# Kernel optimization log

Hardware: AMD Instinct MI355X
Metric: run time of the kernel (lower is better)

The kernel has to match this reference:

```python
import jax, jax.numpy as jnp
import numpy as np

B, T, H, IN = 256, 1024, 512, 1

def setup_inputs() -> dict:
    key = jax.random.key(0)
    ks = jax.random.split(key, 10)
    s = 1.0 / np.sqrt(H)
    return {
        "input": jax.random.normal(ks[0], (B, T), dtype=jnp.float32),
        "Wx0": jax.random.uniform(ks[1], (IN, 4 * H), jnp.float32, -s, s),
        "Wh0": jax.random.uniform(ks[2], (H, 4 * H), jnp.float32, -s, s),
        "b0": jax.random.uniform(ks[3], (4 * H,), jnp.float32, -s, s),
        "Wx1": jax.random.uniform(ks[4], (H, 4 * H), jnp.float32, -s, s),
        "Wh1": jax.random.uniform(ks[5], (H, 4 * H), jnp.float32, -s, s),
        "b1": jax.random.uniform(ks[6], (4 * H,), jnp.float32, -s, s),
        "Wf": jax.random.uniform(ks[7], (H, 1), jnp.float32, -s, s),
        "bf": jax.random.uniform(ks[8], (1,), jnp.float32, -s, s),
    }

def _lstm_layer(xs, Wx, Wh, b):
    # xs: [T, B, in] -> hs: [T, B, H]
    Bd = xs.shape[1]
    Hd = Wh.shape[0]
    h0 = jnp.zeros((Bd, Hd), xs.dtype)
    c0 = jnp.zeros((Bd, Hd), xs.dtype)
    def step(carry, x_t):
        h, c = carry
        g = x_t @ Wx + h @ Wh + b                     # [B, 4H]
        i, f, gg, o = jnp.split(g, 4, axis=-1)
        i = jax.nn.sigmoid(i)
        f = jax.nn.sigmoid(f)
        gg = jnp.tanh(gg)
        o = jax.nn.sigmoid(o)
        c_n = f * c + i * gg
        h_n = o * jnp.tanh(c_n)
        return (h_n, c_n), h_n
    _, hs = jax.lax.scan(step, (h0, c0), xs)
    return hs

def reference(input, Wx0, Wh0, b0, Wx1, Wh1, b1, Wf, bf):
    # input: [B, T] scalar sequence (input_size = 1)
    xs = input.T[:, :, None]                           # [T, B, 1]
    h1 = _lstm_layer(xs, Wx0, Wh0, b0)                 # [T, B, H]
    h2 = _lstm_layer(h1, Wx1, Wh1, b1)                 # [T, B, H]
    out = h2 @ Wf + bf                                 # [T, B, 1]
    return out[:, :, 0].T                              # [B, T]
```

## Files before the change

kernel.cpp:

```cpp
#include <hip/hip_runtime.h>


typedef _Float16 f16;
typedef _Float16 f16x8 __attribute__((ext_vector_type(8)));
typedef float f32x4 __attribute__((ext_vector_type(4)));
typedef unsigned long long u64;

#define NB 256
#define NT_ 1024
#define NH 512
#define RING 16
#define SLOT (NB * NH)

__device__ __forceinline__ float sigm(float x)  { return 1.0f / (1.0f + __expf(-x)); }
__device__ __forceinline__ float tanhx(float x) { return 2.0f / (1.0f + __expf(-2.0f * x)) - 1.0f; }

__device__ __forceinline__ void st8(unsigned short* p, u64 v) {
  __hip_atomic_store((u64*)p, v, __ATOMIC_RELAXED, __HIP_MEMORY_SCOPE_AGENT);
}
__device__ __forceinline__ unsigned ldf(const unsigned* p) {
  return __hip_atomic_load(p, __ATOMIC_RELAXED, __HIP_MEMORY_SCOPE_AGENT);
}
__device__ __forceinline__ unsigned pollr(const unsigned* a, unsigned thr) {
  unsigned v;
  for (;;) {
    v = ldf(a);
    if (!~__ballot(v >= thr)) break;
    __builtin_amdgcn_s_sleep(2);
  }
  asm volatile("" ::: "memory");
  return v;
}

__global__ void prep_xT(const float* __restrict__ inp, float* __restrict__ xT) {
  int g = blockIdx.x * 256 + threadIdx.x;
  int t = g >> 8, b = g & 255;
  xT[t * NB + b] = inp[b * NT_ + t];
}

__global__ void prep_w(const float* __restrict__ Wh0,
                       const float* __restrict__ Wx1,
                       const float* __restrict__ Wh1,
                       f16* __restrict__ dst) {
  int g = blockIdx.x * 256 + threadIdx.x;
  int mat = g >> 20;
  int r = g & 0xFFFFF;
  int j = r & 7, ln = (r >> 3) & 63, kt = (r >> 9) & 15;
  int cl = ln & 15, qd = ln >> 4;
  int k = kt * 32 + qd * 8 + j;
  size_t di; int gcol; const float* W;
  if (mat == 0) {
    int gt = (r >> 13) & 3, nh = (r >> 15) & 1, sl = (r >> 16) & 15;
    W = Wh0;
    gcol = gt * 512 + sl * 32 + nh * 16 + cl;
    di = (size_t)sl * 65536 + (((size_t)(nh * 4 + gt) * 16 + kt) * 64 + ln) * 8 + j;
  } else {
    int jt = (r >> 13) & 1, nh = (r >> 14) & 1, sl = (r >> 15) & 31;
    W = (mat == 1) ? Wx1 : Wh1;
    int gate = jt * 2 + (cl >> 3);
    gcol = gate * 512 + sl * 16 + nh * 8 + (cl & 7);
    di = (size_t)mat * 1048576 + (size_t)sl * 32768 +
         (((size_t)(nh * 2 + jt) * 16 + kt) * 64 + ln) * 8 + j;
  }
  dst[di] = (f16)W[(size_t)k * 2048 + gcol];
}

__global__ void reduce_out(const float* __restrict__ part8,
                           const float* __restrict__ bfp,
                           float* __restrict__ out) {
  int g = blockIdx.x * 256 + threadIdx.x;
  float v = bfp[0];
#pragma unroll
  for (int j = 0; j < 8; ++j) v += part8[(size_t)j * (NB * NT_) + g];
  out[g] = v;
}

__global__ __launch_bounds__(256, 1) void lstm_main(
    const float* __restrict__ xT,
    const f16*  __restrict__ wsl,
    const float* __restrict__ wx0,
    const float* __restrict__ bias0,
    const float* __restrict__ bias1,
    const float* __restrict__ wf,
    unsigned short* p_hi, unsigned short* p_lo,
    unsigned short* q_hi, unsigned short* q_lo,
    unsigned int* pf,
    unsigned int* qf,
    float* part8)
{
  extern __shared__ char smem[];
  const int tid = threadIdx.x;
  const int wv = tid >> 6, ln = tid & 63;
  const int qd = ln >> 4, cl = ln & 15;
  const int bx = blockIdx.x;
  const int r8 = bx & 7, idx = bx >> 3;
  const bool isL0 = !(r8 & 1);
  const int c = r8 >> 1;
  const int sl = idx;
  if (isL0 && idx >= 16) return;
  const float LO = 1.0f / 1024.0f;

  if (isL0) {
    const int4* s0 = (const int4*)wsl + (size_t)sl * 8192;
    int4* d = (int4*)smem;
    for (int i = tid; i < 8192; i += 256) d[i] = s0[i];
  } else {
    const int4* s1 = (const int4*)wsl + 131072 + (size_t)sl * 4096;
    const int4* s2 = (const int4*)wsl + 262144 + (size_t)sl * 4096;
    int4* d = (int4*)smem;
    for (int i = tid; i < 4096; i += 256) { d[i] = s1[i]; d[4096 + i] = s2[i]; }
  }
  __syncthreads();

  unsigned* pfc = pf + c * 32;
  unsigned* qfc = qf + c * 32;

  if (isL0) {
    const int nh = wv >> 1, rhalf = wv & 1;
    const int rb0 = c * 64 + rhalf * 32;
    float wx0v[4], b0c[4];
#pragma unroll
    for (int g = 0; g < 4; ++g) {
      int gc = g * 512 + sl * 32 + nh * 16 + cl;
      wx0v[g] = wx0[gc];
      b0c[g] = bias0[gc];
    }
    float cst[2][4] = {{0.f,0.f,0.f,0.f},{0.f,0.f,0.f,0.f}};
    const bool isq = (ln >= 16 && ln < 48);
    const unsigned* pwa = isq ? (qfc + (ln & 31)) : (pfc + (ln & 15));
    const f16x8* wl = (const f16x8*)smem;
    f16* sh  = (f16*)(smem + 131072);
    f16* slo = sh + 2048;

    for (int s = 0; s < NT_; ++s) {
      if ((s & (RING - 1)) == 0 && s) {
        __syncthreads();
        if (wv == 0)
          asm volatile("buffer_inv sc1\n\ts_waitcnt vmcnt(0)" ::: "memory");
        __syncthreads();
      }
      const int slot_r = (s + RING - 1) & (RING - 1);
      const int slot_w = s & (RING - 1);
      float4 xv[2];
#pragma unroll
      for (int rt = 0; rt < 2; ++rt)
        xv[rt] = *(const float4*)(xT + s * NB + rb0 + rt * 16 + qd * 4);
      if (s) {
        unsigned thr = isq ? (s >= RING ? (unsigned)(s - RING + 1) : 0u)
                           : (unsigned)s;
        pollr(pwa, thr);
      }
      f16x8 Ah[16][2], Al[16][2];
      {
        const f16* bh = (const f16*)p_hi + (size_t)slot_r * SLOT + (size_t)c * 32768 + qd * 8;
        const f16* bl = (const f16*)p_lo + (size_t)slot_r * SLOT + (size_t)c * 32768 + qd * 8;
#pragma unroll
        for (int kt = 0; kt < 16; ++kt)
#pragma unroll
          for (int rt = 0; rt < 2; ++rt) {
            int lr = rhalf * 32 + rt * 16 + cl;
            size_t off = (size_t)kt * 2048 + lr * 32;
            Ah[kt][rt] = *(const f16x8*)(bh + off);
            Al[kt][rt] = *(const f16x8*)(bl + off);
          }
      }
      f32x4 acc[4][2], accL[4][2];
#pragma unroll
      for (int g = 0; g < 4; ++g)
#pragma unroll
        for (int rt = 0; rt < 2; ++rt) {
          acc[g][rt] = (f32x4){0.f,0.f,0.f,0.f};
          accL[g][rt] = (f32x4){0.f,0.f,0.f,0.f};
        }
#pragma unroll
      for (int kt = 0; kt < 16; ++kt) {
#pragma unroll
        for (int g = 0; g < 4; ++g) {
          f16x8 bw = wl[((nh * 4 + g) * 16 + kt) * 64 + ln];
#pragma unroll
          for (int rt = 0; rt < 2; ++rt) {
            acc[g][rt]  = __builtin_amdgcn_mfma_f32_16x16x32_f16(Ah[kt][rt], bw, acc[g][rt], 0, 0, 0);
            accL[g][rt] = __builtin_amdgcn_mfma_f32_16x16x32_f16(Al[kt][rt], bw, accL[g][rt], 0, 0, 0);
          }
        }
      }
#pragma unroll
      for (int rt = 0; rt < 2; ++rt)
#pragma unroll
        for (int e = 0; e < 4; ++e) {
          float xe = (e == 0) ? xv[rt].x : (e == 1) ? xv[rt].y : (e == 2) ? xv[rt].z : xv[rt].w;
          float gi = acc[0][rt][e] + accL[0][rt][e] * LO + xe * wx0v[0] + b0c[0];
          float gf = acc[1][rt][e] + accL[1][rt][e] * LO + xe * wx0v[1] + b0c[1];
          float gg = acc[2][rt][e] + accL[2][rt][e] * LO + xe * wx0v[2] + b0c[2];
          float go = acc[3][rt][e] + accL[3][rt][e] * LO + xe * wx0v[3] + b0c[3];
          float ii = sigm(gi), ff = sigm(gf), tg = tanhx(gg), oo = sigm(go);
          cst[rt][e] = ff * cst[rt][e] + ii * tg;
          float h = oo * tanhx(cst[rt][e]);
          f16 hh = (f16)h;
          int su = (rhalf * 32 + rt * 16 + qd * 4 + e) * 32 + nh * 16 + cl;
          sh[su]  = hh;
          slo[su] = (f16)((h - (float)hh) * 1024.0f);
        }
      __syncthreads();
      {
        unsigned short* bh = p_hi + (size_t)slot_w * SLOT + (size_t)c * 32768 + (size_t)sl * 2048;
        unsigned short* bl = p_lo + (size_t)slot_w * SLOT + (size_t)c * 32768 + (size_t)sl * 2048;
#pragma unroll
        for (int i = tid; i < 1024; i += 256) {
          int strm = i >> 9, pc = i & 511;
          const f16* src = (strm ? slo : sh) + pc * 4;
          st8((strm ? bl : bh) + pc * 4, *(const u64*)src);
        }
      }
      __syncthreads();
      if (tid == 0)
        __hip_atomic_store(pfc + sl, (unsigned)(s + 1),
                           __ATOMIC_RELAXED, __HIP_MEMORY_SCOPE_AGENT);
    }
  } else {
    int u = cl & 7, g01 = cl >> 3;
    const bool hiH = (cl < 8);
    float b1c0[2], b1c1[2], wfv[2];
#pragma unroll
    for (int nh = 0; nh < 2; ++nh) {
      int base = sl * 16 + nh * 8 + u;
      b1c0[nh] = bias1[g01 * 512 + base];
      b1c1[nh] = bias1[(2 + g01) * 512 + base];
      wfv[nh] = wf[base];
    }
    const int lr = wv * 16 + cl;
    float cst[2][4] = {{0.f,0.f,0.f,0.f},{0.f,0.f,0.f,0.f}};
    unsigned pf_seen = 0;
    const f16x8* wx_ = (const f16x8*)smem;
    const f16x8* wh_ = (const f16x8*)(smem + 65536);
    f16* sh  = (f16*)(smem + 131072);
    f16* slo = sh + 1024;

    for (int s = 0; s < NT_; ++s) {
      if ((s & (RING - 1)) == 0 && s) {
        __syncthreads();
        if (wv == 0)
          asm volatile("buffer_inv sc1\n\ts_waitcnt vmcnt(0)" ::: "memory");
        __syncthreads();
      }
      const int slot_r = (s + RING - 1) & (RING - 1);
      const int slot_w = s & (RING - 1);
      if (s) pollr(qfc + (ln & 31), (unsigned)s);
      const f16* aqh = (const f16*)q_hi + (size_t)slot_r * SLOT + (size_t)c * 32768 +
                       (qd >> 1) * 1024 + lr * 16 + (qd & 1) * 8;
      const f16* aql = (const f16*)q_lo + (size_t)slot_r * SLOT + (size_t)c * 32768 +
                       (qd >> 1) * 1024 + lr * 16 + (qd & 1) * 8;
      f16x8 Aq[16][2];
#pragma unroll
      for (int kt = 0; kt < 16; ++kt) {
        Aq[kt][0] = *(const f16x8*)(aqh + kt * 2048);
        Aq[kt][1] = *(const f16x8*)(aql + kt * 2048);
      }
      const f16* aph = (const f16*)p_hi + (size_t)slot_w * SLOT + (size_t)c * 32768 +
                       lr * 32 + qd * 8;
      const f16* apl = (const f16*)p_lo + (size_t)slot_w * SLOT + (size_t)c * 32768 +
                       lr * 32 + qd * 8;
      bool early = __all((int)(pf_seen >= (unsigned)(s + 1)));
      f16x8 Ap[16][2];
      if (early) {
#pragma unroll
        for (int kt = 0; kt < 16; ++kt) {
          Ap[kt][0] = *(const f16x8*)(aph + kt * 2048);
          Ap[kt][1] = *(const f16x8*)(apl + kt * 2048);
        }
      }
      f32x4 acc[4], accL[4];
#pragma unroll
      for (int t4 = 0; t4 < 4; ++t4) {
        acc[t4] = (f32x4){0.f,0.f,0.f,0.f};
        accL[t4] = (f32x4){0.f,0.f,0.f,0.f};
      }
#pragma unroll
      for (int kt = 0; kt < 16; ++kt) {
#pragma unroll
        for (int t4 = 0; t4 < 4; ++t4) {
          f16x8 bw = wh_[(t4 * 16 + kt) * 64 + ln];
          acc[t4]  = __builtin_amdgcn_mfma_f32_16x16x32_f16(Aq[kt][0], bw, acc[t4], 0, 0, 0);
          accL[t4] = __builtin_amdgcn_mfma_f32_16x16x32_f16(Aq[kt][1], bw, accL[t4], 0, 0, 0);
        }
      }
      if (!early) {
        pf_seen = pollr(pfc + (ln & 15), (unsigned)(s + 1));
#pragma unroll
        for (int kt = 0; kt < 16; ++kt) {
          Ap[kt][0] = *(const f16x8*)(aph + kt * 2048);
          Ap[kt][1] = *(const f16x8*)(apl + kt * 2048);
        }
      }
#pragma unroll
      for (int kt = 0; kt < 16; ++kt) {
#pragma unroll
        for (int t4 = 0; t4 < 4; ++t4) {
          f16x8 bw = wx_[(t4 * 16 + kt) * 64 + ln];
          acc[t4]  = __builtin_amdgcn_mfma_f32_16x16x32_f16(Ap[kt][0], bw, acc[t4], 0, 0, 0);
          accL[t4] = __builtin_amdgcn_mfma_f32_16x16x32_f16(Ap[kt][1], bw, accL[t4], 0, 0, 0);
        }
      }
      float po[4];
#pragma unroll
      for (int e = 0; e < 4; ++e) {
        po[e] = 0.0f;
#pragma unroll
        for (int nh = 0; nh < 2; ++nh) {
          float v0 = acc[nh*2+0][e] + accL[nh*2+0][e] * LO + b1c0[nh];
          float v1 = acc[nh*2+1][e] + accL[nh*2+1][e] * LO + b1c1[nh];
          float w0 = __shfl_xor(v0, 8, 16);
          float w1 = __shfl_xor(v1, 8, 16);
          float gi = hiH ? v0 : w0;
          float gf = hiH ? w0 : v0;
          float gg = hiH ? v1 : w1;
          float go = hiH ? w1 : v1;
          float ii = sigm(gi), ff = sigm(gf), tg = tanhx(gg), oo = sigm(go);
          cst[nh][e] = ff * cst[nh][e] + ii * tg;
          float h = oo * tanhx(cst[nh][e]);
          int su = (wv * 16 + qd * 4 + e) * 16 + nh * 8 + u;
          if (hiH) {
            sh[su] = (f16)h;
          } else {
            f16 hh = (f16)h;
            slo[su] = (f16)((h - (float)hh) * 1024.0f);
          }
          po[e] += hiH ? wfv[nh] * h : 0.0f;
        }
      }
      __syncthreads();
      {
        unsigned short* bhq = q_hi + (size_t)slot_w * SLOT + (size_t)c * 32768 + (size_t)sl * 1024;
        unsigned short* blq = q_lo + (size_t)slot_w * SLOT + (size_t)c * 32768 + (size_t)sl * 1024;
#pragma unroll
        for (int i = tid; i < 512; i += 256) {
          int strm = i >> 8, pc = i & 255;
          const f16* src = (strm ? slo : sh) + pc * 4;
          st8((strm ? blq : bhq) + pc * 4, *(const u64*)src);
        }
      }
      __syncthreads();
      if (tid == 0)
        __hip_atomic_store(qfc + sl, (unsigned)(s + 1),
                           __ATOMIC_RELAXED, __HIP_MEMORY_SCOPE_AGENT);
#pragma unroll
      for (int e = 0; e < 4; ++e) {
        float r = po[e];
#pragma unroll
        for (int m = 1; m < 16; m <<= 1) r += __shfl_xor(r, m, 16);
        if (cl == 0)
          atomicAdd(part8 + (size_t)(sl & 7) * (NB * NT_) +
                        (size_t)(c * 64 + wv * 16 + qd * 4 + e) * NT_ + s, r);
      }
    }
  }
}

extern "C" void kernel_launch(void* const* d_in, const int* in_sizes, int n_in,
                              void* d_out, int out_size, void* d_ws, size_t ws_size,
                              hipStream_t stream) {
  (void)in_sizes; (void)n_in; (void)out_size; (void)ws_size;
  const float* inp = (const float*)d_in[0];
  const float* Wx0 = (const float*)d_in[1];
  const float* Wh0 = (const float*)d_in[2];
  const float* b0  = (const float*)d_in[3];
  const float* Wx1 = (const float*)d_in[4];
  const float* Wh1 = (const float*)d_in[5];
  const float* b1  = (const float*)d_in[6];
  const float* Wf  = (const float*)d_in[7];
  const float* bf  = (const float*)d_in[8];

  const size_t MB = 1u << 20;
  const size_t OFF_W    = 0;
  const size_t OFF_XT   = 6 * MB;
  const size_t OFF_PHI  = 7 * MB;
  const size_t OFF_PLO  = 11 * MB;
  const size_t OFF_QHI  = 15 * MB;
  const size_t OFF_QLO  = 19 * MB;
  const size_t OFF_PART = 23 * MB;
  const size_t OFF_CTR  = 31 * MB;

  char* ws = (char*)d_ws;
  f16* wsl = (f16*)(ws + OFF_W);
  float* xT = (float*)(ws + OFF_XT);
  unsigned short* phi = (unsigned short*)(ws + OFF_PHI);
  unsigned short* plo = (unsigned short*)(ws + OFF_PLO);
  unsigned short* qhi = (unsigned short*)(ws + OFF_QHI);
  unsigned short* qlo = (unsigned short*)(ws + OFF_QLO);
  float* part8 = (float*)(ws + OFF_PART);
  unsigned int* pfl = (unsigned int*)(ws + OFF_CTR);
  unsigned int* qfl = pfl + 128;
  float* out = (float*)d_out;

  (void)hipFuncSetAttribute((const void*)lstm_main,
                            hipFuncAttributeMaxDynamicSharedMemorySize, 139264);

  (void)hipMemsetAsync(ws + OFF_PHI, 0, (OFF_CTR + 1024) - OFF_PHI, stream);

  prep_xT<<<1024, 256, 0, stream>>>(inp, xT);
  prep_w<<<12288, 256, 0, stream>>>(Wh0, Wx1, Wh1, wsl);

  lstm_main<<<256, 256, 139264, stream>>>(xT, wsl, Wx0, b0, b1, Wf,
                                          phi, plo, qhi, qlo, pfl, qfl, part8);

  reduce_out<<<1024, 256, 0, stream>>>(part8, bf, out);
}
```

Baseline: 10.29 ms.

## Halve block size to two waves, each computing a larger tile per step

Blocks shrink from four waves to two, and each wave now covers twice as many output tiles. In layer 0 a wave handles both column halves; in layer 1 it handles two row tiles. This reuses each loaded A fragment across more MFMAs and cuts the shared-memory weight reads and block-wide sync participants per step. The cost is much higher register pressure (double the accumulators and A fragments) and half the waves available to hide latency in a step-latency-bound recurrence.

New measurement: 26.61 ms. 159% more time.

```diff
diff --git a/kernel.cpp b/kernel.cpp
--- a/kernel.cpp
+++ b/kernel.cpp
@@ -75,7 +75,7 @@
   out[g] = v;
 }
 
-__global__ __launch_bounds__(256, 1) void lstm_main(
+__global__ __launch_bounds__(128, 1) void lstm_main(
     const float* __restrict__ xT,
     const f16*  __restrict__ wsl,
     const float* __restrict__ wx0,
@@ -103,12 +103,12 @@
   if (isL0) {
     const int4* s0 = (const int4*)wsl + (size_t)sl * 8192;
     int4* d = (int4*)smem;
-    for (int i = tid; i < 8192; i += 256) d[i] = s0[i];
+    for (int i = tid; i < 8192; i += 128) d[i] = s0[i];
   } else {
     const int4* s1 = (const int4*)wsl + 131072 + (size_t)sl * 4096;
     const int4* s2 = (const int4*)wsl + 262144 + (size_t)sl * 4096;
     int4* d = (int4*)smem;
-    for (int i = tid; i < 4096; i += 256) { d[i] = s1[i]; d[4096 + i] = s2[i]; }
+    for (int i = tid; i < 4096; i += 128) { d[i] = s1[i]; d[4096 + i] = s2[i]; }
   }
   __syncthreads();
 
@@ -116,16 +116,17 @@
   unsigned* qfc = qf + c * 32;
 
   if (isL0) {
-    const int nh = wv >> 1, rhalf = wv & 1;
-    const int rb0 = c * 64 + rhalf * 32;
-    float wx0v[4], b0c[4];
-#pragma unroll
-    for (int g = 0; g < 4; ++g) {
-      int gc = g * 512 + sl * 32 + nh * 16 + cl;
-      wx0v[g] = wx0[gc];
-      b0c[g] = bias0[gc];
-    }
-    float cst[2][4] = {{0.f,0.f,0.f,0.f},{0.f,0.f,0.f,0.f}};
+    const int rb0 = c * 64 + wv * 32;
+    float wx0v[2][4], b0c[2][4];
+#pragma unroll
+    for (int nh = 0; nh < 2; ++nh)
+#pragma unroll
+      for (int g = 0; g < 4; ++g) {
+        int gc = g * 512 + sl * 32 + nh * 16 + cl;
+        wx0v[nh][g] = wx0[gc];
+        b0c[nh][g] = bias0[gc];
+      }
+    float cst[2][2][4] = {};
     const bool isq = (ln >= 16 && ln < 48);
     const unsigned* pwa = isq ? (qfc + (ln & 31)) : (pfc + (ln & 15));
     const f16x8* wl = (const f16x8*)smem;
@@ -158,29 +159,29 @@
         for (int kt = 0; kt < 16; ++kt)
 #pragma unroll
           for (int rt = 0; rt < 2; ++rt) {
-            int lr = rhalf * 32 + rt * 16 + cl;
+            int lr = wv * 32 + rt * 16 + cl;
             size_t off = (size_t)kt * 2048 + lr * 32;
             Ah[kt][rt] = *(const f16x8*)(bh + off);
             Al[kt][rt] = *(const f16x8*)(bl + off);
           }
       }
-      f32x4 acc[4][2], accL[4][2];
-#pragma unroll
-      for (int g = 0; g < 4; ++g)
+      f32x4 acc[8][2], accL[8][2];
+#pragma unroll
+      for (int t8 = 0; t8 < 8; ++t8)
 #pragma unroll
         for (int rt = 0; rt < 2; ++rt) {
-          acc[g][rt] = (f32x4){0.f,0.f,0.f,0.f};
-          accL[g][rt] = (f32x4){0.f,0.f,0.f,0.f};
+          acc[t8][rt] = (f32x4){0.f,0.f,0.f,0.f};
+          accL[t8][rt] = (f32x4){0.f,0.f,0.f,0.f};
         }
 #pragma unroll
       for (int kt = 0; kt < 16; ++kt) {
 #pragma unroll
-        for (int g = 0; g < 4; ++g) {
-          f16x8 bw = wl[((nh * 4 + g) * 16 + kt) * 64 + ln];
-#pragma unroll
-          for (int rt = 0; rt < 2; ++rt) {
-            acc[g][rt]  = __builtin_amdgcn_mfma_f32_16x16x32_f16(Ah[kt][rt], bw, acc[g][rt], 0, 0, 0);
-            accL[g][rt] = __builtin_amdgcn_mfma_f32_16x16x32_f16(Al[kt][rt], bw, accL[g][rt], 0, 0, 0);
+        for (int t8 = 0; t8 < 8; ++t8) {
+          f16x8 bw = wl[(t8 * 16 + kt) * 64 + ln];
+#pragma unroll
+          for (int rt = 0; rt < 2; ++rt) {
+            acc[t8][rt]  = __builtin_amdgcn_mfma_f32_16x16x32_f16(Ah[kt][rt], bw, acc[t8][rt], 0, 0, 0);
+            accL[t8][rt] = __builtin_amdgcn_mfma_f32_16x16x32_f16(Al[kt][rt], bw, accL[t8][rt], 0, 0, 0);
           }
         }
       }
@@ -189,24 +190,28 @@
 #pragma unroll
         for (int e = 0; e < 4; ++e) {
           float xe = (e == 0) ? xv[rt].x : (e == 1) ? xv[rt].y : (e == 2) ? xv[rt].z : xv[rt].w;
-          float gi = acc[0][rt][e] + accL[0][rt][e] * LO + xe * wx0v[0] + b0c[0];
-          float gf = acc[1][rt][e] + accL[1][rt][e] * LO + xe * wx0v[1] + b0c[1];
-          float gg = acc[2][rt][e] + accL[2][rt][e] * LO + xe * wx0v[2] + b0c[2];
-          float go = acc[3][rt][e] + accL[3][rt][e] * LO + xe * wx0v[3] + b0c[3];
-          float ii = sigm(gi), ff = sigm(gf), tg = tanhx(gg), oo = sigm(go);
-          cst[rt][e] = ff * cst[rt][e] + ii * tg;
-          float h = oo * tanhx(cst[rt][e]);
-          f16 hh = (f16)h;
-          int su = (rhalf * 32 + rt * 16 + qd * 4 + e) * 32 + nh * 16 + cl;
-          sh[su]  = hh;
-          slo[su] = (f16)((h - (float)hh) * 1024.0f);
+          int r = wv * 32 + rt * 16 + qd * 4 + e;
+#pragma unroll
+          for (int nh = 0; nh < 2; ++nh) {
+            float gi = acc[nh*4+0][rt][e] + accL[nh*4+0][rt][e] * LO + xe * wx0v[nh][0] + b0c[nh][0];
+            float gf = acc[nh*4+1][rt][e] + accL[nh*4+1][rt][e] * LO + xe * wx0v[nh][1] + b0c[nh][1];
+            float gg = acc[nh*4+2][rt][e] + accL[nh*4+2][rt][e] * LO + xe * wx0v[nh][2] + b0c[nh][2];
+            float go = acc[nh*4+3][rt][e] + accL[nh*4+3][rt][e] * LO + xe * wx0v[nh][3] + b0c[nh][3];
+            float ii = sigm(gi), ff = sigm(gf), tg = tanhx(gg), oo = sigm(go);
+            cst[nh][rt][e] = ff * cst[nh][rt][e] + ii * tg;
+            float h = oo * tanhx(cst[nh][rt][e]);
+            f16 hh = (f16)h;
+            int su = r * 32 + nh * 16 + cl;
+            sh[su]  = hh;
+            slo[su] = (f16)((h - (float)hh) * 1024.0f);
+          }
         }
       __syncthreads();
       {
         unsigned short* bh = p_hi + (size_t)slot_w * SLOT + (size_t)c * 32768 + (size_t)sl * 2048;
         unsigned short* bl = p_lo + (size_t)slot_w * SLOT + (size_t)c * 32768 + (size_t)sl * 2048;
 #pragma unroll
-        for (int i = tid; i < 1024; i += 256) {
+        for (int i = tid; i < 1024; i += 128) {
           int strm = i >> 9, pc = i & 511;
           const f16* src = (strm ? slo : sh) + pc * 4;
           st8((strm ? bl : bh) + pc * 4, *(const u64*)src);
@@ -228,8 +233,7 @@
       b1c1[nh] = bias1[(2 + g01) * 512 + base];
       wfv[nh] = wf[base];
     }
-    const int lr = wv * 16 + cl;
-    float cst[2][4] = {{0.f,0.f,0.f,0.f},{0.f,0.f,0.f,0.f}};
+    float cst[2][2][4] = {};
     unsigned pf_seen = 0;
     const f16x8* wx_ = (const f16x8*)smem;
     const f16x8* wh_ = (const f16x8*)(smem + 65536);
@@ -246,94 +250,117 @@
       const int slot_r = (s + RING - 1) & (RING - 1);
       const int slot_w = s & (RING - 1);
       if (s) pollr(qfc + (ln & 31), (unsigned)s);
-      const f16* aqh = (const f16*)q_hi + (size_t)slot_r * SLOT + (size_t)c * 32768 +
-                       (qd >> 1) * 1024 + lr * 16 + (qd & 1) * 8;
-      const f16* aql = (const f16*)q_lo + (size_t)slot_r * SLOT + (size_t)c * 32768 +
-                       (qd >> 1) * 1024 + lr * 16 + (qd & 1) * 8;
-      f16x8 Aq[16][2];
-#pragma unroll
-      for (int kt = 0; kt < 16; ++kt) {
-        Aq[kt][0] = *(const f16x8*)(aqh + kt * 2048);
-        Aq[kt][1] = *(const f16x8*)(aql + kt * 2048);
-      }
-      const f16* aph = (const f16*)p_hi + (size_t)slot_w * SLOT + (size_t)c * 32768 +
-                       lr * 32 + qd * 8;
-      const f16* apl = (const f16*)p_lo + (size_t)slot_w * SLOT + (size_t)c * 32768 +
-                       lr * 32 + qd * 8;
+      f16x8 AqH[16][2], AqL[16][2];
+      {
+        const f16* bq = (const f16*)q_hi + (size_t)slot_r * SLOT + (size_t)c * 32768 +
+                        (qd >> 1) * 1024 + (qd & 1) * 8;
+        const f16* bql = (const f16*)q_lo + (size_t)slot_r * SLOT + (size_t)c * 32768 +
+                         (qd >> 1) * 1024 + (qd & 1) * 8;
+#pragma unroll
+        for (int kt = 0; kt < 16; ++kt)
+#pragma unroll
+          for (int rt = 0; rt < 2; ++rt) {
+            int lr = wv * 32 + rt * 16 + cl;
+            size_t off = (size_t)kt * 2048 + lr * 16;
+            AqH[kt][rt] = *(const f16x8*)(bq + off);
+            AqL[kt][rt] = *(const f16x8*)(bql + off);
+          }
+      }
+      const f16* bp  = (const f16*)p_hi + (size_t)slot_w * SLOT + (size_t)c * 32768 + qd * 8;
+      const f16* bpl = (const f16*)p_lo + (size_t)slot_w * SLOT + (size_t)c * 32768 + qd * 8;
       bool early = __all((int)(pf_seen >= (unsigned)(s + 1)));
-      f16x8 Ap[16][2];
+      f16x8 ApH[16][2], ApL[16][2];
       if (early) {
 #pragma unroll
-        for (int kt = 0; kt < 16; ++kt) {
-          Ap[kt][0] = *(const f16x8*)(aph + kt * 2048);
-          Ap[kt][1] = *(const f16x8*)(apl + kt * 2048);
-        }
-      }
-      f32x4 acc[4], accL[4];
-#pragma unroll
-      for (int t4 = 0; t4 < 4; ++t4) {
-        acc[t4] = (f32x4){0.f,0.f,0.f,0.f};
-        accL[t4] = (f32x4){0.f,0.f,0.f,0.f};
-      }
+        for (int kt = 0; kt < 16; ++kt)
+#pragma unroll
+          for (int rt = 0; rt < 2; ++rt) {
+            int lr = wv * 32 + rt * 16 + cl;
+            size_t off = (size_t)kt * 2048 + lr * 32;
+            ApH[kt][rt] = *(const f16x8*)(bp + off);
+            ApL[kt][rt] = *(const f16x8*)(bpl + off);
+          }
+      }
+      f32x4 acc[4][2], accL[4][2];
+#pragma unroll
+      for (int t4 = 0; t4 < 4; ++t4)
+#pragma unroll
+        for (int rt = 0; rt < 2; ++rt) {
+          acc[t4][rt] = (f32x4){0.f,0.f,0.f,0.f};
+          accL[t4][rt] = (f32x4){0.f,0.f,0.f,0.f};
+        }
 #pragma unroll
       for (int kt = 0; kt < 16; ++kt) {
 #pragma unroll
         for (int t4 = 0; t4 < 4; ++t4) {
           f16x8 bw = wh_[(t4 * 16 + kt) * 64 + ln];
-          acc[t4]  = __builtin_amdgcn_mfma_f32_16x16x32_f16(Aq[kt][0], bw, acc[t4], 0, 0, 0);
-          accL[t4] = __builtin_amdgcn_mfma_f32_16x16x32_f16(Aq[kt][1], bw, accL[t4], 0, 0, 0);
+#pragma unroll
+          for (int rt = 0; rt < 2; ++rt) {
+            acc[t4][rt]  = __builtin_amdgcn_mfma_f32_16x16x32_f16(AqH[kt][rt], bw, acc[t4][rt], 0, 0, 0);
+            accL[t4][rt] = __builtin_amdgcn_mfma_f32_16x16x32_f16(AqL[kt][rt], bw, accL[t4][rt], 0, 0, 0);
+          }
         }
       }
       if (!early) {
         pf_seen = pollr(pfc + (ln & 15), (unsigned)(s + 1));
 #pragma unroll
-        for (int kt = 0; kt < 16; ++kt) {
-          Ap[kt][0] = *(const f16x8*)(aph + kt * 2048);
-          Ap[kt][1] = *(const f16x8*)(apl + kt * 2048);
-        }
+        for (int kt = 0; kt < 16; ++kt)
+#pragma unroll
+          for (int rt = 0; rt < 2; ++rt) {
+            int lr = wv * 32 + rt * 16 + cl;
+            size_t off = (size_t)kt * 2048 + lr * 32;
+            ApH[kt][rt] = *(const f16x8*)(bp + off);
+            ApL[kt][rt] = *(const f16x8*)(bpl + off);
+          }
       }
 #pragma unroll
       for (int kt = 0; kt < 16; ++kt) {
 #pragma unroll
         for (int t4 = 0; t4 < 4; ++t4) {
           f16x8 bw = wx_[(t4 * 16 + kt) * 64 + ln];
-          acc[t4]  = __builtin_amdgcn_mfma_f32_16x16x32_f16(Ap[kt][0], bw, acc[t4], 0, 0, 0);
-          accL[t4] = __builtin_amdgcn_mfma_f32_16x16x32_f16(Ap[kt][1], bw, accL[t4], 0, 0, 0);
-        }
-      }
-      float po[4];
-#pragma unroll
-      for (int e = 0; e < 4; ++e) {
-        po[e] = 0.0f;
-#pragma unroll
-        for (int nh = 0; nh < 2; ++nh) {
-          float v0 = acc[nh*2+0][e] + accL[nh*2+0][e] * LO + b1c0[nh];
-          float v1 = acc[nh*2+1][e] + accL[nh*2+1][e] * LO + b1c1[nh];
-          float w0 = __shfl_xor(v0, 8, 16);
-          float w1 = __shfl_xor(v1, 8, 16);
-          float gi = hiH ? v0 : w0;
-          float gf = hiH ? w0 : v0;
-          float gg = hiH ? v1 : w1;
-          float go = hiH ? w1 : v1;
-          float ii = sigm(gi), ff = sigm(gf), tg = tanhx(gg), oo = sigm(go);
-          cst[nh][e] = ff * cst[nh][e] + ii * tg;
-          float h = oo * tanhx(cst[nh][e]);
-          int su = (wv * 16 + qd * 4 + e) * 16 + nh * 8 + u;
-          if (hiH) {
-            sh[su] = (f16)h;
-          } else {
-            f16 hh = (f16)h;
-            slo[su] = (f16)((h - (float)hh) * 1024.0f);
-          }
-          po[e] += hiH ? wfv[nh] * h : 0.0f;
-        }
-      }
+#pragma unroll
+          for (int rt = 0; rt < 2; ++rt) {
+            acc[t4][rt]  = __builtin_amdgcn_mfma_f32_16x16x32_f16(ApH[kt][rt], bw, acc[t4][rt], 0, 0, 0);
+            accL[t4][rt] = __builtin_amdgcn_mfma_f32_16x16x32_f16(ApL[kt][rt], bw, accL[t4][rt], 0, 0, 0);
+          }
+        }
+      }
+      float po[2][4];
+#pragma unroll
+      for (int rt = 0; rt < 2; ++rt)
+#pragma unroll
+        for (int e = 0; e < 4; ++e) {
+          po[rt][e] = 0.0f;
+          int r = wv * 32 + rt * 16 + qd * 4 + e;
+#pragma unroll
+          for (int nh = 0; nh < 2; ++nh) {
+            float v0 = acc[nh*2+0][rt][e] + accL[nh*2+0][rt][e] * LO + b1c0[nh];
+            float v1 = acc[nh*2+1][rt][e] + accL[nh*2+1][rt][e] * LO + b1c1[nh];
+            float w0 = __shfl_xor(v0, 8, 16);
+            float w1 = __shfl_xor(v1, 8, 16);
+            float gi = hiH ? v0 : w0;
+            float gf = hiH ? w0 : v0;
+            float gg = hiH ? v1 : w1;
+            float go = hiH ? w1 : v1;
+            float ii = sigm(gi), ff = sigm(gf), tg = tanhx(gg), oo = sigm(go);
+            cst[nh][rt][e] = ff * cst[nh][rt][e] + ii * tg;
+            float h = oo * tanhx(cst[nh][rt][e]);
+            int su = r * 16 + nh * 8 + u;
+            if (hiH) {
+              sh[su] = (f16)h;
+            } else {
+              f16 hh = (f16)h;
+              slo[su] = (f16)((h - (float)hh) * 1024.0f);
+            }
+            po[rt][e] += hiH ? wfv[nh] * h : 0.0f;
+          }
+        }
       __syncthreads();
       {
         unsigned short* bhq = q_hi + (size_t)slot_w * SLOT + (size_t)c * 32768 + (size_t)sl * 1024;
         unsigned short* blq = q_lo + (size_t)slot_w * SLOT + (size_t)c * 32768 + (size_t)sl * 1024;
 #pragma unroll
-        for (int i = tid; i < 512; i += 256) {
+        for (int i = tid; i < 512; i += 128) {
           int strm = i >> 8, pc = i & 255;
           const f16* src = (strm ? slo : sh) + pc * 4;
           st8((strm ? blq : bhq) + pc * 4, *(const u64*)src);
@@ -344,14 +371,16 @@
         __hip_atomic_store(qfc + sl, (unsigned)(s + 1),
                            __ATOMIC_RELAXED, __HIP_MEMORY_SCOPE_AGENT);
 #pragma unroll
-      for (int e = 0; e < 4; ++e) {
-        float r = po[e];
-#pragma unroll
-        for (int m = 1; m < 16; m <<= 1) r += __shfl_xor(r, m, 16);
-        if (cl == 0)
-          atomicAdd(part8 + (size_t)(sl & 7) * (NB * NT_) +
-                        (size_t)(c * 64 + wv * 16 + qd * 4 + e) * NT_ + s, r);
-      }
+      for (int rt = 0; rt < 2; ++rt)
+#pragma unroll
+        for (int e = 0; e < 4; ++e) {
+          float r = po[rt][e];
+#pragma unroll
+          for (int m = 1; m < 16; m <<= 1) r += __shfl_xor(r, m, 16);
+          if (cl == 0)
+            atomicAdd(part8 + (size_t)(sl & 7) * (NB * NT_) +
+                          (size_t)(c * 64 + wv * 32 + rt * 16 + qd * 4 + e) * NT_ + s, r);
+        }
     }
   }
 }
@@ -400,7 +429,7 @@
   prep_xT<<<1024, 256, 0, stream>>>(inp, xT);
   prep_w<<<12288, 256, 0, stream>>>(Wh0, Wx1, Wh1, wsl);
 
-  lstm_main<<<256, 256, 139264, stream>>>(xT, wsl, Wx0, b0, b1, Wf,
+  lstm_main<<<256, 128, 139264, stream>>>(xT, wsl, Wx0, b0, b1, Wf,
                                           phi, plo, qhi, qlo, pfl, qfl, part8);
 
   reduce_out<<<1024, 256, 0, stream>>>(part8, bf, out);
```
